# Performance work log

Hardware: AMD Instinct MI355X
Metric: run time of the kernel (lower is better)

## Reference

```python
import jax, jax.numpy as jnp
import numpy as np

INPUT_DIM = 128
HIDDEN_DIM = 128
WINDOW_SIZE = 256
BLOCK_SIZE = 256
BATCH = 8
SEQ = 8192


def setup_inputs() -> dict:
    key = jax.random.key(0)
    ks = jax.random.split(key, 7)
    s = 1.0 / np.sqrt(INPUT_DIM)
    return {
        "x": jax.random.normal(ks[0], (BATCH, SEQ, INPUT_DIM), dtype=jnp.float32),
        "Wq": jax.random.normal(ks[1], (HIDDEN_DIM, INPUT_DIM), dtype=jnp.float32) * s,
        "bq": jax.random.normal(ks[2], (HIDDEN_DIM,), dtype=jnp.float32) * s,
        "Wk": jax.random.normal(ks[3], (HIDDEN_DIM, INPUT_DIM), dtype=jnp.float32) * s,
        "bk": jax.random.normal(ks[4], (HIDDEN_DIM,), dtype=jnp.float32) * s,
        "Wv": jax.random.normal(ks[5], (HIDDEN_DIM, INPUT_DIM), dtype=jnp.float32) * s,
        "bv": jax.random.normal(ks[6], (HIDDEN_DIM,), dtype=jnp.float32) * s,
    }


def reference(x, Wq, bq, Wk, bk, Wv, bv):
    B, S, D = x.shape
    bs, w = BLOCK_SIZE, WINDOW_SIZE
    nb = S // bs
    halo = w - 1
    W = bs + 2 * halo  # per-block K/V window width

    q = x @ Wq.T + bq  # [B,S,H]
    k = x @ Wk.T + bk
    v = x @ Wv.T + bv

    # Zero-pad K/V by halo on both sides. Since there is NO softmax, padded
    # zero keys give zero scores and padded zero values contribute zero —
    # this exactly reproduces the torch code's clamped window slicing.
    k_pad = jnp.pad(k, ((0, 0), (halo, halo), (0, 0)))
    v_pad = jnp.pad(v, ((0, 0), (halo, halo), (0, 0)))

    # Gather overlapping windows: [B, nb, W, H]
    starts = jnp.arange(nb) * bs  # window start in padded coords
    idx = starts[:, None] + jnp.arange(W)[None, :]  # [nb, W]
    k_win = k_pad[:, idx, :]
    v_win = v_pad[:, idx, :]

    q_blk = q.reshape(B, nb, bs, -1)  # [B, nb, bs, H]

    scale = 1.0 / jnp.sqrt(jnp.float32(D))
    attn = jnp.einsum('bnqh,bnkh->bnqk', q_blk, k_win) * scale  # no softmax
    out = jnp.einsum('bnqk,bnkh->bnqh', attn, v_win)
    return out.reshape(B, S, -1)
```

## Files before the change

kernel.cpp:

```cpp
#include <hip/hip_runtime.h>
#include <stdint.h>


#define B_ 8
#define S_ 8192

using bf16x8 = __attribute__((ext_vector_type(8))) short;
using s16x4  = __attribute__((ext_vector_type(4))) short;
using f32x16 = __attribute__((ext_vector_type(16))) float;

__device__ __forceinline__ short f2bf(float f) {
  union { float f; uint32_t u; } v; v.f = f;
  uint32_t r = v.u + 0x7fffu + ((v.u >> 16) & 1u);
  return (short)(r >> 16);
}

#define LDW 136

__global__ __launch_bounds__(256) void proj_kernel(
    const float* __restrict__ x,
    const float* __restrict__ Wq, const float* __restrict__ bq,
    const float* __restrict__ Wk, const float* __restrict__ bk,
    const float* __restrict__ Wv, const float* __restrict__ bv,
    short* __restrict__ qb, short* __restrict__ ktb, short* __restrict__ vtb)
{
  __shared__ short wl[128 * LDW];

  const int tid  = threadIdx.x;
  const int lane = tid & 63;
  const int wv   = tid >> 6;
  const int c    = lane & 31;
  const int hl   = lane >> 5;
  const int r0   = blockIdx.x * 128;
  const int b    = r0 >> 13;
  const int s0   = r0 & (S_ - 1);

  bf16x8 afrag[8];
  {
    const float* xrow = x + (size_t)(r0 + wv * 32 + c) * 128 + hl * 8;
    #pragma unroll
    for (int kst = 0; kst < 8; ++kst) {
      const float4* p = (const float4*)(xrow + kst * 16);
      float4 f0 = p[0], f1 = p[1];
      bf16x8 a;
      a[0] = f2bf(f0.x); a[1] = f2bf(f0.y); a[2] = f2bf(f0.z); a[3] = f2bf(f0.w);
      a[4] = f2bf(f1.x); a[5] = f2bf(f1.y); a[6] = f2bf(f1.z); a[7] = f2bf(f1.w);
      afrag[kst] = a;
    }
  }

  auto stageW = [&](const float* W) {
    #pragma unroll
    for (int it = 0; it < 16; ++it) {
      int l  = it * 256 + tid;
      int n  = l >> 5;
      int k4 = (l & 31) << 2;
      const float4 f = *(const float4*)(W + n * 128 + k4);
      s16x4 o;
      o[0] = f2bf(f.x); o[1] = f2bf(f.y); o[2] = f2bf(f.z); o[3] = f2bf(f.w);
      *(s16x4*)(wl + n * LDW + k4) = o;
    }
  };

  auto gemm = [&](const float* bias, f32x16* acc) {
    #pragma unroll
    for (int nt = 0; nt < 4; ++nt) {
      float bvv = bias[nt * 32 + c];
      #pragma unroll
      for (int i = 0; i < 16; ++i) acc[nt][i] = bvv;
    }
    #pragma unroll
    for (int kst = 0; kst < 8; ++kst) {
      #pragma unroll
      for (int nt = 0; nt < 4; ++nt) {
        bf16x8 bb = *(const bf16x8*)(wl + (nt * 32 + c) * LDW + kst * 16 + hl * 8);
        acc[nt] = __builtin_amdgcn_mfma_f32_32x32x16_bf16(afrag[kst], bb, acc[nt], 0, 0, 0);
      }
    }
  };

  auto writeTransposedLDS = [&](f32x16* acc) {
    #pragma unroll
    for (int nt = 0; nt < 4; ++nt) {
      int d = nt * 32 + c;
      #pragma unroll
      for (int g = 0; g < 4; ++g) {
        #pragma unroll
        for (int p = 0; p < 2; ++p) {
          int reg = g * 4 + p * 2;
          int sl  = wv * 32 + g * 8 + hl * 4 + p * 2;
          uint32_t pk = (uint32_t)(uint16_t)f2bf(acc[nt][reg]) |
                        ((uint32_t)(uint16_t)f2bf(acc[nt][reg + 1]) << 16);
          *(uint32_t*)(wl + d * LDW + sl) = pk;
        }
      }
    }
  };

  auto storeTransposed = [&](short* dst) {
    #pragma unroll
    for (int it = 0; it < 8; ++it) {
      int l  = it * 256 + tid;
      int d  = l >> 4;
      int s8 = (l & 15) << 3;
      bf16x8 vv = *(const bf16x8*)(wl + d * LDW + s8);
      *(bf16x8*)(dst + ((size_t)b * 128 + d) * S_ + s0 + s8) = vv;
    }
  };

  stageW(Wq);
  __syncthreads();
  {
    f32x16 acc[4];
    gemm(bq, acc);
    short* qrow = qb + (size_t)r0 * 128;
    #pragma unroll
    for (int nt = 0; nt < 4; ++nt) {
      #pragma unroll
      for (int reg = 0; reg < 16; ++reg) {
        int row = (reg & 3) + 8 * (reg >> 2) + 4 * hl;
        qrow[(size_t)(wv * 32 + row) * 128 + nt * 32 + c] = f2bf(acc[nt][reg]);
      }
    }
  }
  __syncthreads();

  stageW(Wk);
  __syncthreads();
  {
    f32x16 acc[4];
    gemm(bk, acc);
    __syncthreads();
    writeTransposedLDS(acc);
    __syncthreads();
    storeTransposed(ktb);
  }
  __syncthreads();

  stageW(Wv);
  __syncthreads();
  {
    f32x16 acc[4];
    gemm(bv, acc);
    __syncthreads();
    writeTransposedLDS(acc);
    __syncthreads();
    storeTransposed(vtb);
  }
}

#define LDC 72
#define LDM 136

__global__ __launch_bounds__(256) void attn_kernel(
    const short* __restrict__ qb, const short* __restrict__ ktb,
    const short* __restrict__ vtb, float* __restrict__ out)
{
  __shared__ short smem[2 * 128 * LDC];
  short* kt_c = smem;
  short* vt_c = smem + 128 * LDC;
  short* m_l  = smem;

  const int tid  = threadIdx.x;
  const int lane = tid & 63;
  const int wv   = tid >> 6;
  const int c    = lane & 31;
  const int hl   = lane >> 5;
  const int bn   = blockIdx.x;
  const int b    = bn >> 5;
  const int n    = bn & 31;

  const int win_lo = max(n * 256 - 255, 0);
  const int win_hi = min(n * 256 + 511, S_);

  const short* ktb_b = ktb + (size_t)b * 128 * S_;
  const short* vtb_b = vtb + (size_t)b * 128 * S_;

  f32x16 macc[4];
  #pragma unroll
  for (int nt = 0; nt < 4; ++nt)
    #pragma unroll
    for (int i = 0; i < 16; ++i) macc[nt][i] = 0.f;

  for (int j = 0; j < 12; ++j) {
    int c0 = n * 256 - 256 + j * 64;
    if (c0 + 64 <= win_lo || c0 >= win_hi) continue;
    __syncthreads();
    #pragma unroll
    for (int it = 0; it < 4; ++it) {
      int l  = it * 256 + tid;
      int d  = l >> 3;
      int s8 = (l & 7) << 3;
      int sb = c0 + s8;
      bf16x8 kv = *(const bf16x8*)(ktb_b + (size_t)d * S_ + sb);
      if (sb < win_lo || sb + 7 >= win_hi) {
        #pragma unroll
        for (int e = 0; e < 8; ++e)
          if (sb + e < win_lo || sb + e >= win_hi) kv[e] = 0;
      }
      *(bf16x8*)(kt_c + d * LDC + s8) = kv;
      bf16x8 vv = *(const bf16x8*)(vtb_b + (size_t)d * S_ + sb);
      *(bf16x8*)(vt_c + d * LDC + s8) = vv;
    }
    __syncthreads();
    #pragma unroll
    for (int kst = 0; kst < 4; ++kst) {
      bf16x8 a = *(const bf16x8*)(vt_c + (wv * 32 + c) * LDC + kst * 16 + hl * 8);
      #pragma unroll
      for (int nt = 0; nt < 4; ++nt) {
        bf16x8 bb = *(const bf16x8*)(kt_c + (nt * 32 + c) * LDC + kst * 16 + hl * 8);
        macc[nt] = __builtin_amdgcn_mfma_f32_32x32x16_bf16(a, bb, macc[nt], 0, 0, 0);
      }
    }
  }

  __syncthreads();
  const float scale = 0.08838834764831845f;
  #pragma unroll
  for (int nt = 0; nt < 4; ++nt) {
    #pragma unroll
    for (int reg = 0; reg < 16; ++reg) {
      int row = (reg & 3) + 8 * (reg >> 2) + 4 * hl;
      m_l[(wv * 32 + row) * LDM + nt * 32 + c] = f2bf(macc[nt][reg] * scale);
    }
  }
  __syncthreads();

  f32x16 oacc[2][4];
  #pragma unroll
  for (int mt = 0; mt < 2; ++mt)
    #pragma unroll
    for (int nt = 0; nt < 4; ++nt)
      #pragma unroll
      for (int i = 0; i < 16; ++i) oacc[mt][nt][i] = 0.f;

  const short* q0p = qb + ((size_t)b * S_ + n * 256 + wv * 64 + c) * 128 + hl * 8;
  #pragma unroll
  for (int kst = 0; kst < 8; ++kst) {
    bf16x8 a0 = *(const bf16x8*)(q0p + kst * 16);
    bf16x8 a1 = *(const bf16x8*)(q0p + (size_t)32 * 128 + kst * 16);
    #pragma unroll
    for (int nt = 0; nt < 4; ++nt) {
      bf16x8 bb = *(const bf16x8*)(m_l + (nt * 32 + c) * LDM + kst * 16 + hl * 8);
      oacc[0][nt] = __builtin_amdgcn_mfma_f32_32x32x16_bf16(a0, bb, oacc[0][nt], 0, 0, 0);
      oacc[1][nt] = __builtin_amdgcn_mfma_f32_32x32x16_bf16(a1, bb, oacc[1][nt], 0, 0, 0);
    }
  }

  float* outb = out + ((size_t)b * S_ + n * 256 + wv * 64) * 128;
  #pragma unroll
  for (int mt = 0; mt < 2; ++mt) {
    #pragma unroll
    for (int nt = 0; nt < 4; ++nt) {
      #pragma unroll
      for (int reg = 0; reg < 16; ++reg) {
        int row = mt * 32 + (reg & 3) + 8 * (reg >> 2) + 4 * hl;
        outb[(size_t)row * 128 + nt * 32 + c] = oacc[mt][nt][reg];
      }
    }
  }
}

extern "C" void kernel_launch(void* const* d_in, const int* in_sizes, int n_in,
                              void* d_out, int out_size, void* d_ws, size_t ws_size,
                              hipStream_t stream) {
  const float* x  = (const float*)d_in[0];
  const float* Wq = (const float*)d_in[1];
  const float* bq = (const float*)d_in[2];
  const float* Wk = (const float*)d_in[3];
  const float* bk = (const float*)d_in[4];
  const float* Wv = (const float*)d_in[5];
  const float* bv = (const float*)d_in[6];
  float* out = (float*)d_out;

  const size_t elems = (size_t)B_ * S_ * 128;
  short* qb  = (short*)d_ws;
  short* ktb = qb + elems;
  short* vtb = ktb + elems;

  proj_kernel<<<512, 256, 0, stream>>>(x, Wq, bq, Wk, bk, Wv, bv, qb, ktb, vtb);
  attn_kernel<<<256, 256, 0, stream>>>(qb, ktb, vtb, out);
}
```

Baseline: 134.7 us.

## Double-buffer K/V chunks, widen attention blocks, coalesce Q and output stores

The projection kernel now stages Q through LDS so it can be written with 16-byte vector stores instead of scattered 2-byte stores. The attention kernel moves to 512 threads with 8 waves and splits the V^T·K accumulation across wave pairs. It double-buffers the K/V chunk loads in LDS with register prefetch so global loads overlap the MFMAs, and it computes the loop bounds up front instead of skipping chunks inside the loop. Output is staged through an LDS patch so it can be written as coalesced float4 stores. LDS use per block goes up, and each wave keeps fewer accumulators.

After: 123.6 us. 1.09x faster.

```diff
diff --git a/kernel.cpp b/kernel.cpp
--- a/kernel.cpp
+++ b/kernel.cpp
@@ -113,14 +113,23 @@
   {
     f32x16 acc[4];
     gemm(bq, acc);
-    short* qrow = qb + (size_t)r0 * 128;
+    __syncthreads();
     #pragma unroll
     for (int nt = 0; nt < 4; ++nt) {
       #pragma unroll
       for (int reg = 0; reg < 16; ++reg) {
         int row = (reg & 3) + 8 * (reg >> 2) + 4 * hl;
-        qrow[(size_t)(wv * 32 + row) * 128 + nt * 32 + c] = f2bf(acc[nt][reg]);
-      }
+        wl[(wv * 32 + row) * LDW + nt * 32 + c] = f2bf(acc[nt][reg]);
+      }
+    }
+    __syncthreads();
+    #pragma unroll
+    for (int it = 0; it < 8; ++it) {
+      int l  = it * 256 + tid;
+      int s  = l >> 4;
+      int d8 = (l & 15) << 3;
+      bf16x8 vv = *(const bf16x8*)(wl + s * LDW + d8);
+      *(bf16x8*)(qb + (size_t)(r0 + s) * 128 + d8) = vv;
     }
   }
   __syncthreads();
@@ -151,112 +160,155 @@
 
 #define LDC 72
 #define LDM 136
-
-__global__ __launch_bounds__(256) void attn_kernel(
+#define BUFB 36864
+
+__global__ __launch_bounds__(512) void attn_kernel(
     const short* __restrict__ qb, const short* __restrict__ ktb,
     const short* __restrict__ vtb, float* __restrict__ out)
 {
-  __shared__ short smem[2 * 128 * LDC];
-  short* kt_c = smem;
-  short* vt_c = smem + 128 * LDC;
-  short* m_l  = smem;
+  __shared__ __align__(16) char smem[2 * BUFB + BUFB];
+  short* m_l  = (short*)smem;
+  float* opat = (float*)(smem + 2 * BUFB);
 
   const int tid  = threadIdx.x;
   const int lane = tid & 63;
   const int wv   = tid >> 6;
   const int c    = lane & 31;
   const int hl   = lane >> 5;
-  const int bn   = blockIdx.x;
-  const int b    = bn >> 5;
-  const int n    = bn & 31;
-
-  const int win_lo = max(n * 256 - 255, 0);
-  const int win_hi = min(n * 256 + 511, S_);
+  const int b    = blockIdx.x >> 5;
+  const int n    = blockIdx.x & 31;
+
+  const int win_lo = (n == 0) ? 0 : n * 256 - 255;
+  const int win_hi = (n == 31) ? S_ : n * 256 + 511;
+  const int jlo = (n == 0) ? 4 : 0;
+  const int jhi = (n == 31) ? 8 : 12;
+  const int cbase = n * 256 - 256;
 
   const short* ktb_b = ktb + (size_t)b * 128 * S_;
   const short* vtb_b = vtb + (size_t)b * 128 * S_;
 
-  f32x16 macc[4];
-  #pragma unroll
-  for (int nt = 0; nt < 4; ++nt)
-    #pragma unroll
-    for (int i = 0; i < 16; ++i) macc[nt][i] = 0.f;
-
-  for (int j = 0; j < 12; ++j) {
-    int c0 = n * 256 - 256 + j * 64;
-    if (c0 + 64 <= win_lo || c0 >= win_hi) continue;
-    __syncthreads();
-    #pragma unroll
-    for (int it = 0; it < 4; ++it) {
-      int l  = it * 256 + tid;
-      int d  = l >> 3;
-      int s8 = (l & 7) << 3;
-      int sb = c0 + s8;
-      bf16x8 kv = *(const bf16x8*)(ktb_b + (size_t)d * S_ + sb);
-      if (sb < win_lo || sb + 7 >= win_hi) {
+  const int ht = wv >> 1;
+  const int dh = wv & 1;
+
+  const int sd  = tid >> 3;
+  const int ss8 = (tid & 7) << 3;
+
+  f32x16 macc[2];
+  #pragma unroll
+  for (int ntl = 0; ntl < 2; ++ntl)
+    #pragma unroll
+    for (int i = 0; i < 16; ++i) macc[ntl][i] = 0.f;
+
+  auto loadChunk = [&](int c0, bf16x8* pk, bf16x8* pv) {
+    #pragma unroll
+    for (int it = 0; it < 2; ++it) {
+      int d  = sd + it * 64;
+      int sb = c0 + ss8;
+      pk[it] = *(const bf16x8*)(ktb_b + (size_t)d * S_ + sb);
+      pv[it] = *(const bf16x8*)(vtb_b + (size_t)d * S_ + sb);
+    }
+  };
+
+  auto storeChunk = [&](int c0, short* buf, bf16x8* pk, bf16x8* pv) {
+    short* ktc = buf;
+    short* vtc = buf + 128 * LDC;
+    int sb = c0 + ss8;
+    bool edge = (sb < win_lo) || (sb + 7 >= win_hi);
+    #pragma unroll
+    for (int it = 0; it < 2; ++it) {
+      bf16x8 kv = pk[it];
+      if (edge) {
         #pragma unroll
         for (int e = 0; e < 8; ++e)
           if (sb + e < win_lo || sb + e >= win_hi) kv[e] = 0;
       }
-      *(bf16x8*)(kt_c + d * LDC + s8) = kv;
-      bf16x8 vv = *(const bf16x8*)(vtb_b + (size_t)d * S_ + sb);
-      *(bf16x8*)(vt_c + d * LDC + s8) = vv;
-    }
-    __syncthreads();
+      int d = sd + it * 64;
+      *(bf16x8*)(ktc + d * LDC + ss8) = kv;
+      *(bf16x8*)(vtc + d * LDC + ss8) = pv[it];
+    }
+  };
+
+  auto mfmaChunk = [&](short* buf) {
+    short* ktc = buf;
+    short* vtc = buf + 128 * LDC;
     #pragma unroll
     for (int kst = 0; kst < 4; ++kst) {
-      bf16x8 a = *(const bf16x8*)(vt_c + (wv * 32 + c) * LDC + kst * 16 + hl * 8);
-      #pragma unroll
-      for (int nt = 0; nt < 4; ++nt) {
-        bf16x8 bb = *(const bf16x8*)(kt_c + (nt * 32 + c) * LDC + kst * 16 + hl * 8);
-        macc[nt] = __builtin_amdgcn_mfma_f32_32x32x16_bf16(a, bb, macc[nt], 0, 0, 0);
-      }
-    }
-  }
-
-  __syncthreads();
+      bf16x8 a = *(const bf16x8*)(vtc + (ht * 32 + c) * LDC + kst * 16 + hl * 8);
+      #pragma unroll
+      for (int ntl = 0; ntl < 2; ++ntl) {
+        int nt = dh * 2 + ntl;
+        bf16x8 bb = *(const bf16x8*)(ktc + (nt * 32 + c) * LDC + kst * 16 + hl * 8);
+        macc[ntl] = __builtin_amdgcn_mfma_f32_32x32x16_bf16(a, bb, macc[ntl], 0, 0, 0);
+      }
+    }
+  };
+
+  {
+    bf16x8 pk[2], pv[2];
+    loadChunk(cbase + jlo * 64, pk, pv);
+    storeChunk(cbase + jlo * 64, (short*)smem, pk, pv);
+  }
+  __syncthreads();
+
+  for (int j = jlo; j < jhi; ++j) {
+    short* cur = (short*)(smem + (size_t)(((j - jlo) & 1) ? BUFB : 0));
+    short* nxt = (short*)(smem + (size_t)(((j - jlo) & 1) ? 0 : BUFB));
+    bf16x8 pk[2], pv[2];
+    const bool more = (j + 1 < jhi);
+    if (more) loadChunk(cbase + (j + 1) * 64, pk, pv);
+    mfmaChunk(cur);
+    if (more) storeChunk(cbase + (j + 1) * 64, nxt, pk, pv);
+    __syncthreads();
+  }
+
+  bf16x8 qf[8];
+  {
+    const short* q0p = qb + ((size_t)b * S_ + n * 256 + wv * 32 + c) * 128 + hl * 8;
+    #pragma unroll
+    for (int kst = 0; kst < 8; ++kst) qf[kst] = *(const bf16x8*)(q0p + kst * 16);
+  }
+
   const float scale = 0.08838834764831845f;
   #pragma unroll
-  for (int nt = 0; nt < 4; ++nt) {
+  for (int ntl = 0; ntl < 2; ++ntl) {
     #pragma unroll
     for (int reg = 0; reg < 16; ++reg) {
       int row = (reg & 3) + 8 * (reg >> 2) + 4 * hl;
-      m_l[(wv * 32 + row) * LDM + nt * 32 + c] = f2bf(macc[nt][reg] * scale);
-    }
-  }
-  __syncthreads();
-
-  f32x16 oacc[2][4];
-  #pragma unroll
-  for (int mt = 0; mt < 2; ++mt)
-    #pragma unroll
-    for (int nt = 0; nt < 4; ++nt)
-      #pragma unroll
-      for (int i = 0; i < 16; ++i) oacc[mt][nt][i] = 0.f;
-
-  const short* q0p = qb + ((size_t)b * S_ + n * 256 + wv * 64 + c) * 128 + hl * 8;
+      m_l[(ht * 32 + row) * LDM + (dh * 2 + ntl) * 32 + c] =
+          f2bf(macc[ntl][reg] * scale);
+    }
+  }
+  __syncthreads();
+
+  f32x16 oacc[4];
+  #pragma unroll
+  for (int nt = 0; nt < 4; ++nt)
+    #pragma unroll
+    for (int i = 0; i < 16; ++i) oacc[nt][i] = 0.f;
+
   #pragma unroll
   for (int kst = 0; kst < 8; ++kst) {
-    bf16x8 a0 = *(const bf16x8*)(q0p + kst * 16);
-    bf16x8 a1 = *(const bf16x8*)(q0p + (size_t)32 * 128 + kst * 16);
     #pragma unroll
     for (int nt = 0; nt < 4; ++nt) {
       bf16x8 bb = *(const bf16x8*)(m_l + (nt * 32 + c) * LDM + kst * 16 + hl * 8);
-      oacc[0][nt] = __builtin_amdgcn_mfma_f32_32x32x16_bf16(a0, bb, oacc[0][nt], 0, 0, 0);
-      oacc[1][nt] = __builtin_amdgcn_mfma_f32_32x32x16_bf16(a1, bb, oacc[1][nt], 0, 0, 0);
-    }
-  }
-
-  float* outb = out + ((size_t)b * S_ + n * 256 + wv * 64) * 128;
-  #pragma unroll
-  for (int mt = 0; mt < 2; ++mt) {
-    #pragma unroll
-    for (int nt = 0; nt < 4; ++nt) {
-      #pragma unroll
-      for (int reg = 0; reg < 16; ++reg) {
-        int row = mt * 32 + (reg & 3) + 8 * (reg >> 2) + 4 * hl;
-        outb[(size_t)row * 128 + nt * 32 + c] = oacc[mt][nt][reg];
-      }
+      oacc[nt] = __builtin_amdgcn_mfma_f32_32x32x16_bf16(qf[kst], bb, oacc[nt], 0, 0, 0);
+    }
+  }
+
+  float* patch = opat + wv * (32 * 36);
+  float* outb  = out + ((size_t)b * S_ + n * 256 + wv * 32) * 128;
+  #pragma unroll
+  for (int nt = 0; nt < 4; ++nt) {
+    #pragma unroll
+    for (int reg = 0; reg < 16; ++reg) {
+      int row = (reg & 3) + 8 * (reg >> 2) + 4 * hl;
+      patch[row * 36 + c] = oacc[nt][reg];
+    }
+    #pragma unroll
+    for (int p = 0; p < 4; ++p) {
+      int row = p * 8 + (lane >> 3);
+      float4 vv = *(const float4*)(patch + row * 36 + (lane & 7) * 4);
+      *(float4*)(outb + (size_t)row * 128 + nt * 32 + (lane & 7) * 4) = vv;
     }
   }
 }
@@ -279,5 +331,5 @@
   short* vtb = ktb + elems;
 
   proj_kernel<<<512, 256, 0, stream>>>(x, Wq, bq, Wk, bk, Wv, bv, qb, ktb, vtb);
-  attn_kernel<<<256, 256, 0, stream>>>(qb, ktb, vtb, out);
+  attn_kernel<<<256, 512, 0, stream>>>(qb, ktb, vtb, out);
 }
```
